# Performance work log

Measured on AMD Instinct MI355X. Metric: run time of the kernel, lower is better.

The kernel has to match this reference:

```python
import jax, jax.numpy as jnp
import numpy as np

B, L, D, K, J = 8, 2048, 1024, 32, 512


def setup_inputs() -> dict:
    key = jax.random.key(0)
    ks = jax.random.split(key, 12)
    w = lambda k: jax.random.normal(k, (D, D), jnp.float32) * 0.02
    z = jnp.zeros((D,), jnp.float32)
    return {
        "seg0": jax.random.normal(ks[0], (B, L, D), jnp.float32),
        "seg1": jax.random.normal(ks[1], (B, L, D), jnp.float32),
        "prompt_embed": jax.random.normal(ks[2], (1, 1, D), jnp.float32),
        "Wq_mem": w(ks[3]), "bq_mem": z,
        "Wk_mem": w(ks[4]), "bk_mem": z,
        "Wq": w(ks[5]), "bq": z,
        "Wk": w(ks[6]), "bk": z,
        "Wv": w(ks[7]), "bv": z,
        "Wo": w(ks[8]), "bo": z,
    }


def reference(seg0, seg1, prompt_embed, Wq_mem, bq_mem, Wk_mem, bk_mem,
              Wq, bq, Wk, bk, Wv, bv, Wo, bo):
    scale = 1.0 / np.sqrt(D).astype(np.float32)  # n_heads=1 so d_k = d_model

    def backbone(X):  # single-head SDPA, X: [B, S, D]
        Q = X @ Wq + bq
        Kh = X @ Wk + bk
        V = X @ Wv + bv
        scores = jnp.einsum('bqd,bkd->bqk', Q, Kh) * scale
        attn = jax.nn.softmax(scores, axis=-1)
        out = jnp.einsum('bqk,bkd->bqd', attn, V)
        return out @ Wo + bo

    def summarize(H):  # -> [B, 1, D]
        T = jnp.broadcast_to(prompt_embed, (H.shape[0], 1, D))
        inp = jnp.concatenate([T, H[:, :J, :], T], axis=1)  # [B, J+2, D]
        return backbone(inp)[:, J:J + 1, :]

    # ---- segment 1: memory bank empty -> retrieval is zeros ----
    P0 = jnp.zeros((B, 1, D), seg0.dtype)
    input_h0 = jnp.concatenate([P0, seg0, P0], axis=1)  # [B, L+2, D]
    H_out0 = backbone(input_h0)[:, K + 1:L + K + 2, :]   # clamped slice -> [B, 2017, D]
    out0 = H_out0[:, :-1, :]                             # [B, 2016, D]
    M1 = H_out0[:, -1, :]                                # [B, D] stored memory
    prev_sensory = seg0[:, -K:, :]                       # [B, K, D]

    # ---- segment 2: soft retrieval over 1-entry memory bank ----
    S1 = summarize(seg1)                                 # [B, 1, D]
    M_past = M1[None]                                    # [1, B, D]
    Qn = S1 @ Wq_mem + bq_mem                            # [B, 1, D]
    Kp = M_past @ Wk_mem + bk_mem                        # [1, B, D]
    scores = jnp.matmul(Qn, jnp.swapaxes(Kp, -2, -1)) * scale  # [B, 1, B]
    attn = jax.nn.softmax(scores, axis=-1)
    P1 = jnp.matmul(attn, M_past)                        # [B, 1, D]

    input_h1 = jnp.concatenate([prev_sensory, P1, seg1, P1], axis=1)  # [B, K+L+2, D]
    H_out1 = backbone(input_h1)[:, K + 1:L + K + 2, :]   # [B, 2049, D]
    out1 = H_out1[:, :-1, :]                             # [B, 2048, D]
    return (out0, out1)
```

## Files before the change

kernel.cpp:

```cpp
#include <hip/hip_runtime.h>
#include <stdint.h>
#include <stddef.h>

#define DIM    1024
#define NBATCH 8
#define SEQL   2048
#define JSUM   512
#define SPMAX  2304
#define SPS    768

typedef unsigned long long ull;
typedef __attribute__((ext_vector_type(8))) __bf16 bf16x8;
typedef __attribute__((ext_vector_type(8))) short  short8;
typedef __attribute__((ext_vector_type(4))) float  floatx4;

__device__ __forceinline__ short f2bf(float f) {
  unsigned u = __builtin_bit_cast(unsigned, f);
  u = (u + 0x7fffu + ((u >> 16) & 1u)) >> 16;
  return (short)u;
}
__device__ __forceinline__ float bf2f(short s) {
  unsigned u = ((unsigned)(unsigned short)s) << 16;
  return __builtin_bit_cast(float, u);
}

__device__ __forceinline__ void glds16(const short* g, short8* l) {
  __builtin_amdgcn_global_load_lds(
      (const __attribute__((address_space(1))) unsigned int*)g,
      (__attribute__((address_space(3))) unsigned int*)l, 16, 0, 0);
}

#define VMCNT(n) do { asm volatile("s_waitcnt vmcnt(" #n ")" ::: "memory"); \
                      __builtin_amdgcn_sched_barrier(0); } while (0)

__device__ __forceinline__ void barrier_raw() {
  asm volatile("" ::: "memory");
  __builtin_amdgcn_s_barrier();
  asm volatile("" ::: "memory");
}

struct GemmP {
  const short* A; ull sA; int ldA;
  const short* B; ull sB; int ldB;
  short* C; ull sC;
  int N, Kd;
  const float* bias;
  float* dst0; int t_lo, t_hi, outT;
  float* dstSp; int t_sp, Spad;
  int gx;
  int nblk;
};

template<int MODE, int SWIZ>
__global__ __launch_bounds__(512, 2)
void gemm_nt(GemmP q0, GemmP q1)
{
  const int  pid = blockIdx.x;
  const bool s1  = pid >= q0.nblk;
  const GemmP& q = s1 ? q1 : q0;
  const int  lid = s1 ? (pid - q0.nblk) : pid;

  int tn, tm, bz;
  if (SWIZ == 1) {
    bz = lid & 7;
    const int s = lid >> 3;
    tn = s % q.gx;
    tm = s / q.gx;
  } else {
    tm = lid % q.gx;
    tn = lid / q.gx;
    bz = 0;
  }

  const short* A  = q.A + (ull)bz * q.sA;
  const short* Bm = q.B + (ull)bz * q.sB;

  const int tid  = threadIdx.x;
  const int wave = tid >> 6, lane = tid & 63;

  __shared__ short8 ldsA[2][2048];
  __shared__ short8 ldsB[2][2048];

  const int r0  = tid & 255;
  const int k80 = tid >> 8;
  const short* pA = A  + (long long)(tm * 256 + r0) * q.ldA + k80 * 8;
  const short* pB = Bm + (long long)(tn * 256 + r0) * q.ldB + k80 * 8;

  floatx4 acc[8][4];
#pragma unroll
  for (int i = 0; i < 8; i++)
#pragma unroll
    for (int j = 0; j < 4; j++) acc[i][j] = (floatx4)(0.0f);

  const int wm = (wave >> 2) * 128;
  const int wn = (wave & 3) * 64;
  const int fr = lane & 15;
  const int fq = lane >> 4;

  const int nt = q.Kd >> 6;

  glds16(pA,      &ldsA[0][tid]);
  glds16(pA + 16, &ldsA[0][tid + 512]);
  glds16(pB,      &ldsB[0][tid]);
  glds16(pB + 16, &ldsB[0][tid + 512]);
  glds16(pA + 32, &ldsA[0][1024 + tid]);
  glds16(pA + 48, &ldsA[0][1024 + tid + 512]);
  glds16(pB + 32, &ldsB[0][1024 + tid]);
  glds16(pB + 48, &ldsB[0][1024 + tid + 512]);
  VMCNT(4);
  barrier_raw();

  for (int t = 0; t < nt; t++) {
    const short8* LA = ldsA[t & 1];
    const short8* LB = ldsB[t & 1];
    const int  nb   = (t + 1) & 1;
    const int  koff = (t + 1) * 64;
    const bool stg  = (t + 1) < nt;

    bf16x8 af[4], bv[4];

    {
      const int ka = fq * 256;
#pragma unroll
      for (int mt = 0; mt < 4; mt++)
        af[mt] = __builtin_bit_cast(bf16x8, LA[ka + wm + mt * 16 + fr]);
#pragma unroll
      for (int n2 = 0; n2 < 4; n2++)
        bv[n2] = __builtin_bit_cast(bf16x8, LB[ka + wn + n2 * 16 + fr]);
      if (stg) {
        glds16(pA + koff,      &ldsA[nb][tid]);
        glds16(pA + koff + 16, &ldsA[nb][tid + 512]);
      }
      barrier_raw();
      __builtin_amdgcn_s_setprio(1);
#pragma unroll
      for (int mt = 0; mt < 4; mt++)
#pragma unroll
        for (int n2 = 0; n2 < 4; n2++)
          acc[mt][n2] = __builtin_amdgcn_mfma_f32_16x16x32_bf16(
              af[mt], bv[n2], acc[mt][n2], 0, 0, 0);
      __builtin_amdgcn_s_setprio(0);
      barrier_raw();
    }

    {
      const int ka = fq * 256;
#pragma unroll
      for (int mt = 0; mt < 4; mt++)
        af[mt] = __builtin_bit_cast(bf16x8, LA[ka + wm + 64 + mt * 16 + fr]);
      if (stg) {
        glds16(pB + koff,      &ldsB[nb][tid]);
        glds16(pB + koff + 16, &ldsB[nb][tid + 512]);
      }
      barrier_raw();
      __builtin_amdgcn_s_setprio(1);
#pragma unroll
      for (int mt = 0; mt < 4; mt++)
#pragma unroll
        for (int n2 = 0; n2 < 4; n2++)
          acc[4 + mt][n2] = __builtin_amdgcn_mfma_f32_16x16x32_bf16(
              af[mt], bv[n2], acc[4 + mt][n2], 0, 0, 0);
      __builtin_amdgcn_s_setprio(0);
      if (stg) VMCNT(4); else VMCNT(0);
      barrier_raw();
    }

    {
      const int ka = (fq + 4) * 256;
#pragma unroll
      for (int mt = 0; mt < 4; mt++)
        af[mt] = __builtin_bit_cast(bf16x8, LA[ka + wm + mt * 16 + fr]);
#pragma unroll
      for (int n2 = 0; n2 < 4; n2++)
        bv[n2] = __builtin_bit_cast(bf16x8, LB[ka + wn + n2 * 16 + fr]);
      if (stg) {
        glds16(pA + koff + 32, &ldsA[nb][1024 + tid]);
        glds16(pA + koff + 48, &ldsA[nb][1024 + tid + 512]);
      }
      barrier_raw();
      __builtin_amdgcn_s_setprio(1);
#pragma unroll
      for (int mt = 0; mt < 4; mt++)
#pragma unroll
        for (int n2 = 0; n2 < 4; n2++)
          acc[mt][n2] = __builtin_amdgcn_mfma_f32_16x16x32_bf16(
              af[mt], bv[n2], acc[mt][n2], 0, 0, 0);
      __builtin_amdgcn_s_setprio(0);
      barrier_raw();
    }

    {
      const int ka = (fq + 4) * 256;
#pragma unroll
      for (int mt = 0; mt < 4; mt++)
        af[mt] = __builtin_bit_cast(bf16x8, LA[ka + wm + 64 + mt * 16 + fr]);
      if (stg) {
        glds16(pB + koff + 32, &ldsB[nb][1024 + tid]);
        glds16(pB + koff + 48, &ldsB[nb][1024 + tid + 512]);
      }
      barrier_raw();
      __builtin_amdgcn_s_setprio(1);
#pragma unroll
      for (int mt = 0; mt < 4; mt++)
#pragma unroll
        for (int n2 = 0; n2 < 4; n2++)
          acc[4 + mt][n2] = __builtin_amdgcn_mfma_f32_16x16x32_bf16(
              af[mt], bv[n2], acc[4 + mt][n2], 0, 0, 0);
      __builtin_amdgcn_s_setprio(0);
      if (stg) VMCNT(4);
      barrier_raw();
    }
  }

  if (MODE == 3) {
    const int bb  = (tm * 256) / q.Spad;
    const int rb0 = tm * 256 - bb * q.Spad + wm + fq * 4;
#pragma unroll
    for (int mf = 0; mf < 8; mf++) {
#pragma unroll
      for (int n2 = 0; n2 < 4; n2++) {
        const int col = tn * 256 + wn + n2 * 16 + fr;
#pragma unroll
        for (int r = 0; r < 4; r++) {
          const int tt = rb0 + (mf >> 2) * 64 + (mf & 3) * 16 + r;
          float v = acc[mf][n2][r] + q.bias[col];
          if (tt >= q.t_lo && tt < q.t_hi)
            q.dst0[((size_t)bb * q.outT + (tt - q.t_lo)) * DIM + col] = v;
          else if (tt == q.t_sp)
            q.dstSp[(size_t)bb * DIM + col] = v;
        }
      }
    }
  } else {
    short* C = q.C + (ull)bz * q.sC;
#pragma unroll
    for (int mf = 0; mf < 8; mf++) {
#pragma unroll
      for (int n2 = 0; n2 < 4; n2++) {
        const int col = tn * 256 + wn + n2 * 16 + fr;
        float bn = (MODE == 1) ? q.bias[col] : 0.0f;
#pragma unroll
        for (int r = 0; r < 4; r++) {
          const int row = tm * 256 + wm + (mf >> 2) * 64 + (mf & 3) * 16 + fq * 4 + r;
          float v = acc[mf][n2][r] + bn;
          if (MODE == 2) v += q.bias[row];
          C[(size_t)row * q.N + col] = f2bf(v);
        }
      }
    }
  }
}

__global__ __launch_bounds__(256)
void softmax_rows2(short* __restrict__ SA0, int Spad0, int S0, int nx0,
                   short* __restrict__ SA1, int Spad1, int S1, float scale)
{
  __shared__ float buf[SPMAX];
  __shared__ float red[8];
  int t = blockIdx.x;
  const int b = blockIdx.y;
  short* row; int Spad, S;
  if (t < nx0) { row = SA0 + ((size_t)b * Spad0 + t) * Spad0; Spad = Spad0; S = S0; }
  else { t -= nx0; row = SA1 + ((size_t)b * Spad1 + t) * Spad1; Spad = Spad1; S = S1; }
  const int tid = threadIdx.x;
  const int nv = S >> 3;

  float mx = -1e30f;
  for (int g = tid; g < nv; g += 256) {
    short8 v = ((const short8*)row)[g];
#pragma unroll
    for (int j = 0; j < 8; j++) {
      float f = bf2f(v[j]) * scale;
      buf[g * 8 + j] = f;
      mx = fmaxf(mx, f);
    }
  }
  for (int i = (nv << 3) + tid; i < S; i += 256) {
    float f = bf2f(row[i]) * scale;
    buf[i] = f;
    mx = fmaxf(mx, f);
  }
  for (int off = 32; off; off >>= 1) mx = fmaxf(mx, __shfl_down(mx, off, 64));
  if ((tid & 63) == 0) red[tid >> 6] = mx;
  __syncthreads();
  if (tid == 0) {
    float m = red[0];
    for (int w = 1; w < 4; w++) m = fmaxf(m, red[w]);
    red[0] = m;
  }
  __syncthreads();
  mx = red[0];

  float sum = 0.f;
  for (int i = tid; i < S; i += 256) {
    float e = __expf(buf[i] - mx);
    buf[i] = e;
    sum += e;
  }
  for (int off = 32; off; off >>= 1) sum += __shfl_down(sum, off, 64);
  if ((tid & 63) == 0) red[4 + (tid >> 6)] = sum;
  __syncthreads();
  if (tid == 0) red[4] = 1.0f / (red[4] + red[5] + red[6] + red[7]);
  __syncthreads();
  const float rinv = red[4];

  for (int g = tid; g < nv; g += 256) {
    short8 o;
#pragma unroll
    for (int j = 0; j < 8; j++) o[j] = f2bf(buf[g * 8 + j] * rinv);
    ((short8*)row)[g] = o;
  }
  for (int i = (nv << 3) + tid; i < S; i += 256) row[i] = f2bf(buf[i] * rinv);
  for (int i = S + tid; i < Spad; i += 256) row[i] = 0;
}

__global__ __launch_bounds__(256)
void wtrans(const float* __restrict__ W, short* __restrict__ WT)
{
  __shared__ float tile[32][33];
  const int bn = blockIdx.x * 32, bk = blockIdx.y * 32;
  const int tx = threadIdx.x & 31, ty = threadIdx.x >> 5;
#pragma unroll
  for (int j = 0; j < 4; j++)
    tile[ty + j * 8][tx] = W[(size_t)(bk + ty + j * 8) * DIM + bn + tx];
  __syncthreads();
#pragma unroll
  for (int j = 0; j < 4; j++)
    WT[(size_t)(bn + ty + j * 8) * DIM + bk + tx] = f2bf(tile[tx][ty + j * 8]);
}

__global__ __launch_bounds__(256)
void bcat(const float* __restrict__ a, const float* __restrict__ b,
          float* __restrict__ o)
{
  const int i = blockIdx.x * 256 + threadIdx.x;
  o[i] = (i < DIM) ? a[i] : b[i - DIM];
}

__global__ __launch_bounds__(256)
void assemble0(const float* __restrict__ seg0, short* __restrict__ X)
{
  const int Spad = SPMAX;
  const int b = blockIdx.y;
  const size_t lin = ((size_t)blockIdx.x * 256 + threadIdx.x) * 4;
  const int t = (int)(lin >> 10), d = (int)(lin & 1023);
  float4 v = make_float4(0.f, 0.f, 0.f, 0.f);
  if (t >= 1 && t <= SEQL)
    v = *(const float4*)(seg0 + ((size_t)b * SEQL + (t - 1)) * DIM + d);
  union { short s[4]; ull u; } o;
  o.s[0] = f2bf(v.x); o.s[1] = f2bf(v.y); o.s[2] = f2bf(v.z); o.s[3] = f2bf(v.w);
  *(ull*)(X + (size_t)b * Spad * DIM + lin) = o.u;
}

__global__ __launch_bounds__(256)
void assembleS(const float* __restrict__ seg1, const float* __restrict__ prompt,
               short* __restrict__ X)
{
  const int Spad = SPS;
  const int b = blockIdx.y;
  const size_t lin = ((size_t)blockIdx.x * 256 + threadIdx.x) * 4;
  const int t = (int)(lin >> 10), d = (int)(lin & 1023);
  float4 v = make_float4(0.f, 0.f, 0.f, 0.f);
  if (t == 0 || t == JSUM + 1)
    v = *(const float4*)(prompt + d);
  else if (t >= 1 && t <= JSUM)
    v = *(const float4*)(seg1 + ((size_t)b * SEQL + (t - 1)) * DIM + d);
  union { short s[4]; ull u; } o;
  o.s[0] = f2bf(v.x); o.s[1] = f2bf(v.y); o.s[2] = f2bf(v.z); o.s[3] = f2bf(v.w);
  *(ull*)(X + (size_t)b * Spad * DIM + lin) = o.u;
}

__global__ __launch_bounds__(256)
void assemble1(const float* __restrict__ seg0, const float* __restrict__ seg1,
               const float* __restrict__ P1, short* __restrict__ X)
{
  const int Spad = SPMAX;
  const int b = blockIdx.y;
  const size_t lin = ((size_t)blockIdx.x * 256 + threadIdx.x) * 4;
  const int t = (int)(lin >> 10), d = (int)(lin & 1023);
  float4 v = make_float4(0.f, 0.f, 0.f, 0.f);
  if (t < 32)
    v = *(const float4*)(seg0 + ((size_t)b * SEQL + (SEQL - 32 + t)) * DIM + d);
  else if (t == 32 || t == 2081)
    v = *(const float4*)(P1 + (size_t)b * DIM + d);
  else if (t >= 33 && t <= 2080)
    v = *(const float4*)(seg1 + ((size_t)b * SEQL + (t - 33)) * DIM + d);
  union { short s[4]; ull u; } o;
  o.s[0] = f2bf(v.x); o.s[1] = f2bf(v.y); o.s[2] = f2bf(v.z); o.s[3] = f2bf(v.w);
  *(ull*)(X + (size_t)b * Spad * DIM + lin) = o.u;
}

__global__ __launch_bounds__(256)
void mem_proj(const float* __restrict__ Sb, const float* __restrict__ M1,
              const float* __restrict__ Wq_mem, const float* __restrict__ bq_mem,
              const float* __restrict__ Wk_mem, const float* __restrict__ bk_mem,
              float* __restrict__ Qn, float* __restrict__ Kp)
{
  const int n = blockIdx.x * 256 + threadIdx.x;
  const int b = blockIdx.y;
  const int w = blockIdx.z;
  const float* x    = w ? M1 : Sb;
  const float* W    = w ? Wk_mem : Wq_mem;
  const float* bias = w ? bk_mem : bq_mem;
  float* o          = w ? Kp : Qn;
  const float* xr = x + (size_t)b * DIM;
  float s = bias[n];
  for (int k = 0; k < DIM; k++) s += xr[k] * W[(size_t)k * DIM + n];
  o[(size_t)b * DIM + n] = s;
}

__global__ __launch_bounds__(256)
void mem_attn(const float* __restrict__ Qn, const float* __restrict__ Kp,
              const float* __restrict__ M1, float* __restrict__ P1, float scale)
{
  __shared__ float red[256];
  __shared__ float w8[8];
  const int b = blockIdx.x, tid = threadIdx.x;
  for (int bp = 0; bp < NBATCH; bp++) {
    float p = 0.f;
    for (int k = tid; k < DIM; k += 256)
      p += Qn[(size_t)b * DIM + k] * Kp[(size_t)bp * DIM + k];
    red[tid] = p; __syncthreads();
    for (int off = 128; off; off >>= 1) {
      if (tid < off) red[tid] += red[tid + off];
      __syncthreads();
    }
    if (tid == 0) w8[bp] = red[0] * scale;
    __syncthreads();
  }
  if (tid == 0) {
    float m = w8[0];
    for (int i = 1; i < NBATCH; i++) m = fmaxf(m, w8[i]);
    float s = 0.f;
    for (int i = 0; i < NBATCH; i++) { w8[i] = __expf(w8[i] - m); s += w8[i]; }
    for (int i = 0; i < NBATCH; i++) w8[i] /= s;
  }
  __syncthreads();
  for (int d = tid; d < DIM; d += 256) {
    float a = 0.f;
    for (int bp = 0; bp < NBATCH; bp++) a += w8[bp] * M1[(size_t)bp * DIM + d];
    P1[(size_t)b * DIM + d] = a;
  }
}

extern "C" void kernel_launch(void* const* d_in, const int* in_sizes, int n_in,
                              void* d_out, int out_size, void* d_ws, size_t ws_size,
                              hipStream_t stream)
{
  const float* seg0   = (const float*)d_in[0];
  const float* seg1   = (const float*)d_in[1];
  const float* prompt = (const float*)d_in[2];
  const float* Wq_mem = (const float*)d_in[3];
  const float* bq_mem = (const float*)d_in[4];
  const float* Wk_mem = (const float*)d_in[5];
  const float* bk_mem = (const float*)d_in[6];
  const float* Wq     = (const float*)d_in[7];
  const float* bq     = (const float*)d_in[8];
  const float* Wk     = (const float*)d_in[9];
  const float* bk     = (const float*)d_in[10];
  const float* Wv     = (const float*)d_in[11];
  const float* bv     = (const float*)d_in[12];
  const float* Wo     = (const float*)d_in[13];
  const float* bo     = (const float*)d_in[14];
  float* outp = (float*)d_out;

  const size_t WSZ   = (size_t)DIM * DIM * 2;
  const size_t XSZ   = (size_t)NBATCH * SPMAX * DIM * 2;
  const size_t SASZ  = (size_t)NBATCH * SPMAX * SPMAX * 2;
  const size_t XSZS  = (size_t)NBATCH * SPS * DIM * 2;
  const size_t SASZS = (size_t)NBATCH * SPS * SPS * 2;
  const size_t VSZ   = (size_t)NBATCH * DIM * 4;

  char* p = (char*)d_ws;
  short* WqT  = (short*)p; p += WSZ;
  short* WkT  = (short*)p; p += WSZ;
  short* WvT  = (short*)p; p += WSZ;
  short* WoT  = (short*)p; p += WSZ;
  short* X    = (short*)p; p += XSZ;
  short* QKb  = (short*)p; p += 2 * XSZ;
  short* Vt   = (short*)p; p += XSZ;
  short* Ctx  = (short*)p; p += XSZ;
  short* SA   = (short*)p; p += SASZ;
  short* XS   = (short*)p; p += XSZS;
  short* QKbS = (short*)p; p += 2 * XSZS;
  short* VtS  = (short*)p; p += XSZS;
  short* CtxS = (short*)p; p += XSZS;
  short* SAS  = (short*)p; p += SASZS;
  float* M1b  = (float*)p; p += VSZ;
  float* Sb   = (float*)p; p += VSZ;
  float* Qn   = (float*)p; p += VSZ;
  float* Kp   = (float*)p; p += VSZ;
  float* P1   = (float*)p; p += VSZ;
  float* bqk  = (float*)p; p += 2 * DIM * 4;

  const float scale = 0.03125f;
  dim3 blk(256, 1, 1);
  dim3 blkG(512, 1, 1);

  auto P = [](const short* A, ull sA, int ldA,
              const short* B, ull sB, int ldB,
              short* C, ull sC, int N, int Kd, const float* bias,
              float* dst0, int t_lo, int t_hi, int outT,
              float* dstSp, int t_sp, int Spad, int gx, int nblk) {
    GemmP q{A, sA, ldA, B, sB, ldB, C, sC, N, Kd, bias,
            dst0, t_lo, t_hi, outT, dstSp, t_sp, Spad, gx, nblk};
    return q;
  };

  wtrans<<<dim3(32, 32), blk, 0, stream>>>(Wq, WqT);
  wtrans<<<dim3(32, 32), blk, 0, stream>>>(Wk, WkT);
  wtrans<<<dim3(32, 32), blk, 0, stream>>>(Wv, WvT);
  wtrans<<<dim3(32, 32), blk, 0, stream>>>(Wo, WoT);
  bcat<<<dim3(8), blk, 0, stream>>>(bq, bk, bqk);

  assemble0<<<dim3(SPMAX, NBATCH), blk, 0, stream>>>(seg0, X);
  assembleS<<<dim3(SPS, NBATCH), blk, 0, stream>>>(seg1, prompt, XS);

  {
    GemmP a = P(X, 0, DIM, WqT, 0, DIM, QKb, 0, 2048, DIM, bqk,
                nullptr, 0, 0, 0, nullptr, -1, SPMAX, NBATCH * SPMAX / 256, 576);
    GemmP b = P(XS, 0, DIM, WqT, 0, DIM, QKbS, 0, 2048, DIM, bqk,
                nullptr, 0, 0, 0, nullptr, -1, SPS, NBATCH * SPS / 256, 192);
    gemm_nt<1, 2><<<dim3(768), blkG, 0, stream>>>(a, b);
  }
  {
    GemmP a = P(WvT, 0, DIM, X, (ull)SPMAX * DIM, DIM,
                Vt, (ull)DIM * SPMAX, SPMAX, DIM, bv,
                nullptr, 0, 0, 0, nullptr, -1, SPMAX, SPMAX / 256, 288);
    GemmP b = P(WvT, 0, DIM, XS, (ull)SPS * DIM, DIM,
                VtS, (ull)DIM * SPS, SPS, DIM, bv,
                nullptr, 0, 0, 0, nullptr, -1, SPS, SPS / 256, 96);
    gemm_nt<2, 1><<<dim3(384), blkG, 0, stream>>>(a, b);
  }
  {
    GemmP a = P(QKb, (ull)SPMAX * 2048, 2048, QKb + DIM, (ull)SPMAX * 2048, 2048,
                SA, (ull)SPMAX * SPMAX, SPMAX, DIM, nullptr,
                nullptr, 0, 0, 0, nullptr, -1, SPMAX, SPMAX / 256, 648);
    GemmP b = P(QKbS, (ull)SPS * 2048, 2048, QKbS + DIM, (ull)SPS * 2048, 2048,
                SAS, (ull)SPS * SPS, SPS, DIM, nullptr,
                nullptr, 0, 0, 0, nullptr, -1, SPS, SPS / 256, 72);
    gemm_nt<0, 1><<<dim3(720), blkG, 0, stream>>>(a, b);
  }
  softmax_rows2<<<dim3(SPMAX + SPS, NBATCH), blk, 0, stream>>>(
      SA, SPMAX, 2050, SPMAX, SAS, SPS, 514, scale);
  {
    GemmP a = P(SA, (ull)SPMAX * SPMAX, SPMAX, Vt, (ull)DIM * SPMAX, SPMAX,
                Ctx, (ull)SPMAX * DIM, DIM, 2112, nullptr,
                nullptr, 0, 0, 0, nullptr, -1, SPMAX, DIM / 256, 288);
    GemmP b = P(SAS, (ull)SPS * SPS, SPS, VtS, (ull)DIM * SPS, SPS,
                CtxS, (ull)SPS * DIM, DIM, 576, nullptr,
                nullptr, 0, 0, 0, nullptr, -1, SPS, DIM / 256, 96);
    gemm_nt<0, 1><<<dim3(384), blkG, 0, stream>>>(a, b);
  }
  {
    GemmP a = P(Ctx, 0, DIM, WoT, 0, DIM, nullptr, 0, DIM, DIM, bo,
                outp, 33, 2049, 2016, M1b, 2049, SPMAX, NBATCH * SPMAX / 256, 288);
    GemmP b = P(CtxS, 0, DIM, WoT, 0, DIM, nullptr, 0, DIM, DIM, bo,
                nullptr, 0, 0, 0, Sb, JSUM, SPS, NBATCH * SPS / 256, 96);
    gemm_nt<3, 2><<<dim3(384), blkG, 0, stream>>>(a, b);
  }

  mem_proj<<<dim3(DIM / 256, NBATCH, 2), blk, 0, stream>>>(
      Sb, M1b, Wq_mem, bq_mem, Wk_mem, bk_mem, Qn, Kp);
  mem_attn<<<dim3(NBATCH), blk, 0, stream>>>(Qn, Kp, M1b, P1, scale);

  assemble1<<<dim3(SPMAX, NBATCH), blk, 0, stream>>>(seg0, seg1, P1, X);
  {
    GemmP a = P(X, 0, DIM, WqT, 0, DIM, QKb, 0, 2048, DIM, bqk,
                nullptr, 0, 0, 0, nullptr, -1, SPMAX, NBATCH * SPMAX / 256, 576);
    gemm_nt<1, 2><<<dim3(576), blkG, 0, stream>>>(a, a);
  }
  {
    GemmP a = P(WvT, 0, DIM, X, (ull)SPMAX * DIM, DIM,
                Vt, (ull)DIM * SPMAX, SPMAX, DIM, bv,
                nullptr, 0, 0, 0, nullptr, -1, SPMAX, SPMAX / 256, 288);
    gemm_nt<2, 1><<<dim3(288), blkG, 0, stream>>>(a, a);
  }
  {
    GemmP a = P(QKb, (ull)SPMAX * 2048, 2048, QKb + DIM, (ull)SPMAX * 2048, 2048,
                SA, (ull)SPMAX * SPMAX, SPMAX, DIM, nullptr,
                nullptr, 0, 0, 0, nullptr, -1, SPMAX, SPMAX / 256, 648);
    gemm_nt<0, 1><<<dim3(648), blkG, 0, stream>>>(a, a);
  }
  softmax_rows2<<<dim3(SPMAX, NBATCH), blk, 0, stream>>>(
      SA, SPMAX, 2082, SPMAX, SA, SPMAX, 2082, scale);
  {
    GemmP a = P(SA, (ull)SPMAX * SPMAX, SPMAX, Vt, (ull)DIM * SPMAX, SPMAX,
                Ctx, (ull)SPMAX * DIM, DIM, 2112, nullptr,
                nullptr, 0, 0, 0, nullptr, -1, SPMAX, DIM / 256, 288);
    gemm_nt<0, 1><<<dim3(288), blkG, 0, stream>>>(a, a);
  }
  {
    GemmP a = P(Ctx, 0, DIM, WoT, 0, DIM, nullptr, 0, DIM, DIM, bo,
                outp + (size_t)NBATCH * 2016 * DIM, 33, 2081, 2048,
                nullptr, -1, SPMAX, NBATCH * SPMAX / 256, 288);
    gemm_nt<3, 2><<<dim3(288), blkG, 0, stream>>>(a, a);
  }
}
```

Baseline: 1.442 ms.

## Halve GEMM mainloop barriers and merge second-segment QK and V projection launches

The GEMM kernel's MODE and SWIZ template parameters become runtime fields in GemmP. This lets the segment-2 QK projection and the V-transpose projection, which use different modes, run as one 864-block launch instead of two. Each of the two k-halves of the main loop now runs as one block with a single trailing barrier instead of two, and B fragments are loaded before A fragments. The aim is less barrier stall and launch overhead and better CU fill. The cost is runtime branches in the epilogue, possible register pressure, and less barrier-enforced interleaving between LDS reads and async global-to-LDS staging.

```diff
diff --git a/kernel.cpp b/kernel.cpp
--- a/kernel.cpp
+++ b/kernel.cpp
@@ -49,9 +49,10 @@
   float* dstSp; int t_sp, Spad;
   int gx;
   int nblk;
+  int mode;
+  int swiz;
 };
 
-template<int MODE, int SWIZ>
 __global__ __launch_bounds__(512, 2)
 void gemm_nt(GemmP q0, GemmP q1)
 {
@@ -61,7 +62,7 @@
   const int  lid = s1 ? (pid - q0.nblk) : pid;
 
   int tn, tm, bz;
-  if (SWIZ == 1) {
+  if (q.swiz == 1) {
     bz = lid & 7;
     const int s = lid >> 3;
     tn = s % q.gx;
@@ -122,16 +123,15 @@
     {
       const int ka = fq * 256;
 #pragma unroll
-      for (int mt = 0; mt < 4; mt++)
-        af[mt] = __builtin_bit_cast(bf16x8, LA[ka + wm + mt * 16 + fr]);
-#pragma unroll
       for (int n2 = 0; n2 < 4; n2++)
         bv[n2] = __builtin_bit_cast(bf16x8, LB[ka + wn + n2 * 16 + fr]);
+#pragma unroll
+      for (int mt = 0; mt < 4; mt++)
+        af[mt] = __builtin_bit_cast(bf16x8, LA[ka + wm + mt * 16 + fr]);
       if (stg) {
         glds16(pA + koff,      &ldsA[nb][tid]);
         glds16(pA + koff + 16, &ldsA[nb][tid + 512]);
       }
-      barrier_raw();
       __builtin_amdgcn_s_setprio(1);
 #pragma unroll
       for (int mt = 0; mt < 4; mt++)
@@ -140,11 +140,6 @@
           acc[mt][n2] = __builtin_amdgcn_mfma_f32_16x16x32_bf16(
               af[mt], bv[n2], acc[mt][n2], 0, 0, 0);
       __builtin_amdgcn_s_setprio(0);
-      barrier_raw();
-    }
-
-    {
-      const int ka = fq * 256;
 #pragma unroll
       for (int mt = 0; mt < 4; mt++)
         af[mt] = __builtin_bit_cast(bf16x8, LA[ka + wm + 64 + mt * 16 + fr]);
@@ -152,7 +147,6 @@
         glds16(pB + koff,      &ldsB[nb][tid]);
         glds16(pB + koff + 16, &ldsB[nb][tid + 512]);
       }
-      barrier_raw();
       __builtin_amdgcn_s_setprio(1);
 #pragma unroll
       for (int mt = 0; mt < 4; mt++)
@@ -168,16 +162,15 @@
     {
       const int ka = (fq + 4) * 256;
 #pragma unroll
-      for (int mt = 0; mt < 4; mt++)
-        af[mt] = __builtin_bit_cast(bf16x8, LA[ka + wm + mt * 16 + fr]);
-#pragma unroll
       for (int n2 = 0; n2 < 4; n2++)
         bv[n2] = __builtin_bit_cast(bf16x8, LB[ka + wn + n2 * 16 + fr]);
+#pragma unroll
+      for (int mt = 0; mt < 4; mt++)
+        af[mt] = __builtin_bit_cast(bf16x8, LA[ka + wm + mt * 16 + fr]);
       if (stg) {
         glds16(pA + koff + 32, &ldsA[nb][1024 + tid]);
         glds16(pA + koff + 48, &ldsA[nb][1024 + tid + 512]);
       }
-      barrier_raw();
       __builtin_amdgcn_s_setprio(1);
 #pragma unroll
       for (int mt = 0; mt < 4; mt++)
@@ -186,11 +179,6 @@
           acc[mt][n2] = __builtin_amdgcn_mfma_f32_16x16x32_bf16(
               af[mt], bv[n2], acc[mt][n2], 0, 0, 0);
       __builtin_amdgcn_s_setprio(0);
-      barrier_raw();
-    }
-
-    {
-      const int ka = (fq + 4) * 256;
 #pragma unroll
       for (int mt = 0; mt < 4; mt++)
         af[mt] = __builtin_bit_cast(bf16x8, LA[ka + wm + 64 + mt * 16 + fr]);
@@ -198,7 +186,6 @@
         glds16(pB + koff + 32, &ldsB[nb][1024 + tid]);
         glds16(pB + koff + 48, &ldsB[nb][1024 + tid + 512]);
       }
-      barrier_raw();
       __builtin_amdgcn_s_setprio(1);
 #pragma unroll
       for (int mt = 0; mt < 4; mt++)
@@ -212,7 +199,7 @@
     }
   }
 
-  if (MODE == 3) {
+  if (q.mode == 3) {
     const int bb  = (tm * 256) / q.Spad;
     const int rb0 = tm * 256 - bb * q.Spad + wm + fq * 4;
 #pragma unroll
@@ -238,12 +225,12 @@
 #pragma unroll
       for (int n2 = 0; n2 < 4; n2++) {
         const int col = tn * 256 + wn + n2 * 16 + fr;
-        float bn = (MODE == 1) ? q.bias[col] : 0.0f;
+        float bn = (q.mode == 1) ? q.bias[col] : 0.0f;
 #pragma unroll
         for (int r = 0; r < 4; r++) {
           const int row = tm * 256 + wm + (mf >> 2) * 64 + (mf & 3) * 16 + fq * 4 + r;
           float v = acc[mf][n2][r] + bn;
-          if (MODE == 2) v += q.bias[row];
+          if (q.mode == 2) v += q.bias[row];
           C[(size_t)row * q.N + col] = f2bf(v);
         }
       }
@@ -501,9 +488,10 @@
               const short* B, ull sB, int ldB,
               short* C, ull sC, int N, int Kd, const float* bias,
               float* dst0, int t_lo, int t_hi, int outT,
-              float* dstSp, int t_sp, int Spad, int gx, int nblk) {
+              float* dstSp, int t_sp, int Spad, int gx, int nblk,
+              int mode, int swiz) {
     GemmP q{A, sA, ldA, B, sB, ldB, C, sC, N, Kd, bias,
-            dst0, t_lo, t_hi, outT, dstSp, t_sp, Spad, gx, nblk};
+            dst0, t_lo, t_hi, outT, dstSp, t_sp, Spad, gx, nblk, mode, swiz};
     return q;
   };
 
@@ -518,46 +506,46 @@
 
   {
     GemmP a = P(X, 0, DIM, WqT, 0, DIM, QKb, 0, 2048, DIM, bqk,
-                nullptr, 0, 0, 0, nullptr, -1, SPMAX, NBATCH * SPMAX / 256, 576);
+                nullptr, 0, 0, 0, nullptr, -1, SPMAX, NBATCH * SPMAX / 256, 576, 1, 2);
     GemmP b = P(XS, 0, DIM, WqT, 0, DIM, QKbS, 0, 2048, DIM, bqk,
-                nullptr, 0, 0, 0, nullptr, -1, SPS, NBATCH * SPS / 256, 192);
-    gemm_nt<1, 2><<<dim3(768), blkG, 0, stream>>>(a, b);
+                nullptr, 0, 0, 0, nullptr, -1, SPS, NBATCH * SPS / 256, 192, 1, 2);
+    gemm_nt<<<dim3(768), blkG, 0, stream>>>(a, b);
   }
   {
     GemmP a = P(WvT, 0, DIM, X, (ull)SPMAX * DIM, DIM,
                 Vt, (ull)DIM * SPMAX, SPMAX, DIM, bv,
-                nullptr, 0, 0, 0, nullptr, -1, SPMAX, SPMAX / 256, 288);
+                nullptr, 0, 0, 0, nullptr, -1, SPMAX, SPMAX / 256, 288, 2, 1);
     GemmP b = P(WvT, 0, DIM, XS, (ull)SPS * DIM, DIM,
                 VtS, (ull)DIM * SPS, SPS, DIM, bv,
-                nullptr, 0, 0, 0, nullptr, -1, SPS, SPS / 256, 96);
-    gemm_nt<2, 1><<<dim3(384), blkG, 0, stream>>>(a, b);
+                nullptr, 0, 0, 0, nullptr, -1, SPS, SPS / 256, 96, 2, 1);
+    gemm_nt<<<dim3(384), blkG, 0, stream>>>(a, b);
   }
   {
     GemmP a = P(QKb, (ull)SPMAX * 2048, 2048, QKb + DIM, (ull)SPMAX * 2048, 2048,
                 SA, (ull)SPMAX * SPMAX, SPMAX, DIM, nullptr,
-                nullptr, 0, 0, 0, nullptr, -1, SPMAX, SPMAX / 256, 648);
+                nullptr, 0, 0, 0, nullptr, -1, SPMAX, SPMAX / 256, 648, 0, 1);
     GemmP b = P(QKbS, (ull)SPS * 2048, 2048, QKbS + DIM, (ull)SPS * 2048, 2048,
                 SAS, (ull)SPS * SPS, SPS, DIM, nullptr,
-                nullptr, 0, 0, 0, nullptr, -1, SPS, SPS / 256, 72);
-    gemm_nt<0, 1><<<dim3(720), blkG, 0, stream>>>(a, b);
+                nullptr, 0, 0, 0, nullptr, -1, SPS, SPS / 256, 72, 0, 1);
+    gemm_nt<<<dim3(720), blkG, 0, stream>>>(a, b);
   }
   softmax_rows2<<<dim3(SPMAX + SPS, NBATCH), blk, 0, stream>>>(
       SA, SPMAX, 2050, SPMAX, SAS, SPS, 514, scale);
   {
     GemmP a = P(SA, (ull)SPMAX * SPMAX, SPMAX, Vt, (ull)DIM * SPMAX, SPMAX,
                 Ctx, (ull)SPMAX * DIM, DIM, 2112, nullptr,
-                nullptr, 0, 0, 0, nullptr, -1, SPMAX, DIM / 256, 288);
+                nullptr, 0, 0, 0, nullptr, -1, SPMAX, DIM / 256, 288, 0, 1);
     GemmP b = P(SAS, (ull)SPS * SPS, SPS, VtS, (ull)DIM * SPS, SPS,
                 CtxS, (ull)SPS * DIM, DIM, 576, nullptr,
-                nullptr, 0, 0, 0, nullptr, -1, SPS, DIM / 256, 96);
-    gemm_nt<0, 1><<<dim3(384), blkG, 0, stream>>>(a, b);
+                nullptr, 0, 0, 0, nullptr, -1, SPS, DIM / 256, 96, 0, 1);
+    gemm_nt<<<dim3(384), blkG, 0, stream>>>(a, b);
   }
   {
     GemmP a = P(Ctx, 0, DIM, WoT, 0, DIM, nullptr, 0, DIM, DIM, bo,
-                outp, 33, 2049, 2016, M1b, 2049, SPMAX, NBATCH * SPMAX / 256, 288);
+                outp, 33, 2049, 2016, M1b, 2049, SPMAX, NBATCH * SPMAX / 256, 288, 3, 2);
     GemmP b = P(CtxS, 0, DIM, WoT, 0, DIM, nullptr, 0, DIM, DIM, bo,
-                nullptr, 0, 0, 0, Sb, JSUM, SPS, NBATCH * SPS / 256, 96);
-    gemm_nt<3, 2><<<dim3(384), blkG, 0, stream>>>(a, b);
+                nullptr, 0, 0, 0, Sb, JSUM, SPS, NBATCH * SPS / 256, 96, 3, 2);
+    gemm_nt<<<dim3(384), blkG, 0, stream>>>(a, b);
   }
 
   mem_proj<<<dim3(DIM / 256, NBATCH, 2), blk, 0, stream>>>(
@@ -567,33 +555,30 @@
   assemble1<<<dim3(SPMAX, NBATCH), blk, 0, stream>>>(seg0, seg1, P1, X);
   {
     GemmP a = P(X, 0, DIM, WqT, 0, DIM, QKb, 0, 2048, DIM, bqk,
-                nullptr, 0, 0, 0, nullptr, -1, SPMAX, NBATCH * SPMAX / 256, 576);
-    gemm_nt<1, 2><<<dim3(576), blkG, 0, stream>>>(a, a);
-  }
-  {
-    GemmP a = P(WvT, 0, DIM, X, (ull)SPMAX * DIM, DIM,
+                nullptr, 0, 0, 0, nullptr, -1, SPMAX, NBATCH * SPMAX / 256, 576, 1, 2);
+    GemmP b = P(WvT, 0, DIM, X, (ull)SPMAX * DIM, DIM,
                 Vt, (ull)DIM * SPMAX, SPMAX, DIM, bv,
-                nullptr, 0, 0, 0, nullptr, -1, SPMAX, SPMAX / 256, 288);
-    gemm_nt<2, 1><<<dim3(288), blkG, 0, stream>>>(a, a);
+                nullptr, 0, 0, 0, nullptr, -1, SPMAX, SPMAX / 256, 288, 2, 1);
+    gemm_nt<<<dim3(864), blkG, 0, stream>>>(a, b);
   }
   {
     GemmP a = P(QKb, (ull)SPMAX * 2048, 2048, QKb + DIM, (ull)SPMAX * 2048, 2048,
                 SA, (ull)SPMAX * SPMAX, SPMAX, DIM, nullptr,
-                nullptr, 0, 0, 0, nullptr, -1, SPMAX, SPMAX / 256, 648);
-    gemm_nt<0, 1><<<dim3(648), blkG, 0, stream>>>(a, a);
+                nullptr, 0, 0, 0, nullptr, -1, SPMAX, SPMAX / 256, 648, 0, 1);
+    gemm_nt<<<dim3(648), blkG, 0, stream>>>(a, a);
   }
   softmax_rows2<<<dim3(SPMAX, NBATCH), blk, 0, stream>>>(
       SA, SPMAX, 2082, SPMAX, SA, SPMAX, 2082, scale);
   {
     GemmP a = P(SA, (ull)SPMAX * SPMAX, SPMAX, Vt, (ull)DIM * SPMAX, SPMAX,
                 Ctx, (ull)SPMAX * DIM, DIM, 2112, nullptr,
-                nullptr, 0, 0, 0, nullptr, -1, SPMAX, DIM / 256, 288);
-    gemm_nt<0, 1><<<dim3(288), blkG, 0, stream>>>(a, a);
+                nullptr, 0, 0, 0, nullptr, -1, SPMAX, DIM / 256, 288, 0, 1);
+    gemm_nt<<<dim3(288), blkG, 0, stream>>>(a, a);
   }
   {
     GemmP a = P(Ctx, 0, DIM, WoT, 0, DIM, nullptr, 0, DIM, DIM, bo,
                 outp + (size_t)NBATCH * 2016 * DIM, 33, 2081, 2048,
-                nullptr, -1, SPMAX, NBATCH * SPMAX / 256, 288);
-    gemm_nt<3, 2><<<dim3(288), blkG, 0, stream>>>(a, a);
-  }
-}
+                nullptr, -1, SPMAX, NBATCH * SPMAX / 256, 288, 3, 2);
+    gemm_nt<<<dim3(288), blkG, 0, stream>>>(a, a);
+  }
+}
```

Result: slower. 1.484 ms (+2.9%).
